# Kernel optimization log

Hardware: AMD Instinct MI355X
Metric: run time of the kernel (lower is better)

## Reference

```python
import jax, jax.numpy as jnp
import numpy as np
from jax import lax

B, T, I, H, G = 128, 1024, 256, 512, 4 * 512


def _lstm_layer(x, W_ih, W_hh, b_ih, b_hh):
    """x: [B, T, in]. Returns (outputs [B, T, H], final_h [B, H]).
    PyTorch gate order: i, f, g, o."""
    Bsz = x.shape[0]
    Hh = W_hh.shape[1]
    # Precompute input contribution to gates for all timesteps: [T, B, 4H]
    xg = jnp.einsum('bti,gi->tbg', x, W_ih) + b_ih + b_hh

    def step(carry, xg_t):
        h, c = carry
        g = xg_t + h @ W_hh.T  # [B, 4H]
        i, f, gg, o = jnp.split(g, 4, axis=-1)
        c = jax.nn.sigmoid(f) * c + jax.nn.sigmoid(i) * jnp.tanh(gg)
        h = jax.nn.sigmoid(o) * jnp.tanh(c)
        return (h, c), h

    zeros = jnp.zeros((Bsz, Hh), dtype=x.dtype)
    (h_T, _), hs = lax.scan(step, (zeros, zeros), xg)
    return jnp.transpose(hs, (1, 0, 2)), h_T


def setup_inputs() -> dict:
    key = jax.random.key(0)
    ks = jax.random.split(key, 11)
    s_in = 1.0 / np.sqrt(H)  # torch LSTM init scale ~ U(-1/sqrt(H), 1/sqrt(H))
    return {
        'x': jax.random.normal(ks[0], (B, T, I), jnp.float32),
        'W_ih0': jax.random.normal(ks[1], (G, I), jnp.float32) * s_in,
        'W_hh0': jax.random.normal(ks[2], (G, H), jnp.float32) * s_in,
        'b_ih0': jax.random.normal(ks[3], (G,), jnp.float32) * s_in,
        'b_hh0': jax.random.normal(ks[4], (G,), jnp.float32) * s_in,
        'W_ih1': jax.random.normal(ks[5], (G, H), jnp.float32) * s_in,
        'W_hh1': jax.random.normal(ks[6], (G, H), jnp.float32) * s_in,
        'b_ih1': jax.random.normal(ks[7], (G,), jnp.float32) * s_in,
        'b_hh1': jax.random.normal(ks[8], (G,), jnp.float32) * s_in,
        'fc_w': jax.random.normal(ks[9], (1, H), jnp.float32) * s_in,
        'fc_b': jax.random.normal(ks[10], (1,), jnp.float32) * s_in,
    }


def reference(x, W_ih0, W_hh0, b_ih0, b_hh0, W_ih1, W_hh1, b_ih1, b_hh1, fc_w, fc_b):
    out0, _ = _lstm_layer(x, W_ih0, W_hh0, b_ih0, b_hh0)
    _, h_last = _lstm_layer(out0, W_ih1, W_hh1, b_ih1, b_hh1)
    # dropout is identity in eval mode (and dropout=0.0)
    logits = h_last @ fc_w.T + fc_b  # [B, 1]
    return logits.squeeze(-1)  # [B]
```

## Files before the change

### kernel.cpp

```cpp
#include <hip/hip_runtime.h>
#include <stdint.h>


#define T_STEPS 1024
#define NBLK 512
#define NTHR 256

#define WS_WP0   0u
#define WS_WP1   3145728u
#define WS_BP0   7340032u
#define WS_BP1   7348224u
#define WS_H     7356416u
#define WS_CNT   8404992u
#define CNT_U32  512

typedef __bf16 bf16x8 __attribute__((ext_vector_type(8)));
typedef float  f32x4  __attribute__((ext_vector_type(4)));
typedef unsigned long long ull;
typedef ull u64x2 __attribute__((ext_vector_type(2)));

__device__ __forceinline__ unsigned short f2bf(float f) {
    union { float f; uint32_t u; } a; a.f = f;
    uint32_t r = a.u + 0x7fffu + ((a.u >> 16) & 1u);
    return (unsigned short)(r >> 16);
}
__device__ __forceinline__ float bf2f(unsigned short u) {
    union { uint32_t u; float f; } a; a.u = ((uint32_t)u) << 16; return a.f;
}
__device__ __forceinline__ float sigm(float x)  { return 1.f / (1.f + __expf(-x)); }
__device__ __forceinline__ float tanh_f(float x){ return 2.f / (1.f + __expf(-2.f * x)) - 1.f; }

__device__ __forceinline__ bf16x8 ld_h16(const unsigned short* p) {
    u64x2 t;
    t.x = __hip_atomic_load((const ull*)p,       __ATOMIC_RELAXED, __HIP_MEMORY_SCOPE_SYSTEM);
    t.y = __hip_atomic_load((const ull*)(p + 4), __ATOMIC_RELAXED, __HIP_MEMORY_SCOPE_SYSTEM);
    return __builtin_bit_cast(bf16x8, t);
}
__device__ __forceinline__ void st_sys_u32(unsigned* p, unsigned v) {
    __hip_atomic_store(p, v, __ATOMIC_RELAXED, __HIP_MEMORY_SCOPE_SYSTEM);
}
__device__ __forceinline__ unsigned ld_sys_u32(const unsigned* p) {
    return __hip_atomic_load(p, __ATOMIC_RELAXED, __HIP_MEMORY_SCOPE_SYSTEM);
}

__global__ void k_pack(const float* __restrict__ Wih0, const float* __restrict__ Whh0,
                       const float* __restrict__ Wih1, const float* __restrict__ Whh1,
                       unsigned short* __restrict__ Wp0, unsigned short* __restrict__ Wp1)
{
    int t = blockIdx.x * blockDim.x + threadIdx.x;
    const int N0 = 2048 * 768;
    const int N1 = 2048 * 1024;
    if (t < N0) {
        int r = t / 768, k = t - r * 768;
        int u = r >> 2, q = r & 3, row = q * 512 + u;
        float v = (k < 256) ? Wih0[row * 256 + k] : Whh0[row * 512 + (k - 256)];
        Wp0[t] = f2bf(v);
    } else if (t < N0 + N1) {
        int t2 = t - N0;
        int r = t2 >> 10, k = t2 & 1023;
        int u = r >> 2, q = r & 3, row = q * 512 + u;
        float v = (k < 512) ? Wih1[row * 512 + k] : Whh1[row * 512 + (k - 512)];
        Wp1[t2] = f2bf(v);
    }
}

__global__ void k_misc(const float* __restrict__ bih0, const float* __restrict__ bhh0,
                       const float* __restrict__ bih1, const float* __restrict__ bhh1,
                       float* __restrict__ bp0, float* __restrict__ bp1,
                       unsigned short* __restrict__ hbufs, unsigned* __restrict__ cnt)
{
    int t = blockIdx.x * blockDim.x + threadIdx.x;
    if (t < 2048) {
        int u = t >> 2, q = t & 3, row = q * 512 + u;
        bp0[t] = bih0[row] + bhh0[row];
    } else if (t < 4096) {
        int r = t - 2048; int u = r >> 2, q = r & 3, row = q * 512 + u;
        bp1[r] = bih1[row] + bhh1[row];
    } else if (t < 4096 + 524288) {
        hbufs[t - 4096] = 0;
    } else if (t < 4096 + 524288 + CNT_U32) {
        cnt[t - (4096 + 524288)] = 0;
    }
}

template<int NKW, int KTOT, int KS, bool L0>
__device__ __forceinline__ void run_layer(
    int b0, int ut0, int g0, int w, int col, int quad, int tid,
    const float* __restrict__ x,
    const unsigned short* __restrict__ Wp,
    const float* __restrict__ bp,
    unsigned short* __restrict__ hb,
    unsigned* slots, int myslot,
    float (*red)[16][68])
{
    const int bA   = b0 + col;
    const int lane = tid & 63;

    uint4 Bf[4][NKW];
    #pragma unroll
    for (int f = 0; f < 4; ++f) {
        const unsigned short* wrow = Wp + (g0 + f * 16 + col) * KTOT + w * (NKW * 32) + quad * 8;
        #pragma unroll
        for (int ks = 0; ks < NKW; ++ks)
            Bf[f][ks] = *(const uint4*)(wrow + ks * 32);
    }
    #pragma unroll
    for (int f = 0; f < 4; ++f) {
        #pragma unroll
        for (int ks = 0; ks < NKW; ++ks) {
            uint32_t c0 = Bf[f][ks].x, c1 = Bf[f][ks].y, c2 = Bf[f][ks].z, c3 = Bf[f][ks].w;
            asm volatile("" : "+v"(c0), "+v"(c1), "+v"(c2), "+v"(c3));
            Bf[f][ks].x = c0; Bf[f][ks].y = c1; Bf[f][ks].z = c2; Bf[f][ks].w = c3;
        }
    }

    const int bl = tid >> 4, ul = tid & 15;
    const f32x4 bias = *(const f32x4*)(bp + g0 + ul * 4);
    float c = 0.f;

    int  offA[NKW];
    bool s0[NKW];
    #pragma unroll
    for (int ks = 0; ks < NKW; ++ks) {
        int kg = w * (NKW * 32) + ks * 32 + quad * 8;
        if (kg < KS) { s0[ks] = true;  offA[ks] = L0 ? (bA * (T_STEPS * 256) + kg) : (bA * 512 + kg); }
        else         { s0[ks] = false; offA[ks] = bA * 512 + (kg - KS); }
    }

    const int SMAX = L0 ? (T_STEPS - 1) : T_STEPS;

    for (int s = 0; s <= SMAX; ++s) {
        const bool active = L0 || (s >= 1);
        bf16x8 Af[NKW];

        if (L0) {
            const float* xb = x + s * 256;
            #pragma unroll
            for (int ks = 0; ks < NKW; ++ks) {
                if (s0[ks]) {
                    const float* p = xb + offA[ks];
                    float4 lo = *(const float4*)p;
                    float4 hi = *(const float4*)(p + 4);
                    bf16x8 v;
                    v[0]=(__bf16)lo.x; v[1]=(__bf16)lo.y; v[2]=(__bf16)lo.z; v[3]=(__bf16)lo.w;
                    v[4]=(__bf16)hi.x; v[5]=(__bf16)hi.y; v[6]=(__bf16)hi.z; v[7]=(__bf16)hi.w;
                    Af[ks] = v;
                }
            }
        }

        if (s >= 1 && tid < 64) {
            int tgt = L0 ? (s - ((lane & 1) << 1)) : s;
            if (lane == myslot) tgt = (int)0x80000000;
            for (;;) {
                int v = (int)ld_sys_u32(slots + lane);
                if (__all(v >= tgt)) break;
                __builtin_amdgcn_s_sleep(1);
            }
        }
        __syncthreads();

        if (active) {
            if (L0) {
                const unsigned short* hr = hb + (((unsigned)(s + 3)) & 3u) * 65536;
                #pragma unroll
                for (int ks = 0; ks < NKW; ++ks)
                    if (!s0[ks]) Af[ks] = ld_h16(hr + offA[ks]);
            } else {
                const unsigned short* h0r = hb + (((unsigned)(s + 3)) & 3u) * 65536;
                const unsigned short* h1r = hb + 262144 + (((unsigned)(s + 2)) & 3u) * 65536;
                #pragma unroll
                for (int ks = 0; ks < NKW; ++ks)
                    Af[ks] = ld_h16((s0[ks] ? h0r : h1r) + offA[ks]);
            }

            f32x4 acc[4] = { f32x4{0,0,0,0}, f32x4{0,0,0,0}, f32x4{0,0,0,0}, f32x4{0,0,0,0} };
            #pragma unroll
            for (int ks = 0; ks < NKW; ++ks) {
                #pragma unroll
                for (int f = 0; f < 4; ++f)
                    acc[f] = __builtin_amdgcn_mfma_f32_16x16x32_bf16(
                        Af[ks], __builtin_bit_cast(bf16x8, Bf[f][ks]), acc[f], 0, 0, 0);
            }
            #pragma unroll
            for (int f = 0; f < 4; ++f) {
                #pragma unroll
                for (int r = 0; r < 4; ++r)
                    red[w][quad * 4 + r][f * 16 + col] = acc[f][r];
            }
        }
        __syncthreads();
        if (active) {
            f32x4 g = bias;
            #pragma unroll
            for (int ww = 0; ww < 4; ++ww)
                g += *(const f32x4*)&red[ww][bl][ul * 4];
            float ig = sigm(g[0]), fg = sigm(g[1]), gc = tanh_f(g[2]), og = sigm(g[3]);
            c = fg * c + ig * gc;
            float h = og * tanh_f(c);
            unsigned short hv = f2bf(h);
            unsigned short pv = (unsigned short)__shfl_xor((int)hv, 1);
            if (!(ul & 1)) {
                unsigned short* hw = L0
                    ? (hb + (((unsigned)s) & 3u) * 65536)
                    : (hb + 262144 + (((unsigned)(s + 3)) & 3u) * 65536);
                unsigned pk = (unsigned)hv | ((unsigned)pv << 16);
                st_sys_u32((unsigned*)(hw + (b0 + bl) * 512 + ut0 + ul), pk);
            }
        }
        asm volatile("s_waitcnt vmcnt(0)" ::: "memory");
        __syncthreads();
        if (tid == 0)
            st_sys_u32(slots + myslot, (unsigned)(s + 1));
    }
}

__global__ __launch_bounds__(NTHR, 2) void lstm_persistent(
    const float* __restrict__ x,
    const unsigned short* __restrict__ Wp0, const unsigned short* __restrict__ Wp1,
    const float* __restrict__ bp0, const float* __restrict__ bp1,
    unsigned short* __restrict__ hb, unsigned* __restrict__ cnt)
{
    __shared__ alignas(16) float red[4][16][68];
    const int bid   = blockIdx.x;
    const int g     = bid & 7;
    const int rest  = bid >> 3;
    const int layer = rest & 1;
    const int ut    = rest >> 1;
    const int b0    = g * 16;
    const int ut0   = ut * 16;
    const int g0    = ut * 64;
    const int tid   = threadIdx.x;
    const int w = tid >> 6, lane = tid & 63, col = lane & 15, quad = lane >> 4;

    unsigned* slots = cnt + g * 64;
    const int myslot = rest;

    if (layer == 0)
        run_layer<6, 768, 256, true >(b0, ut0, g0, w, col, quad, tid, x, Wp0, bp0, hb, slots, myslot, red);
    else
        run_layer<8, 1024, 512, false>(b0, ut0, g0, w, col, quad, tid, x, Wp1, bp1, hb, slots, myslot, red);
}

__global__ void k_fc(const unsigned short* __restrict__ h1, const float* __restrict__ fcw,
                     const float* __restrict__ fcb, float* __restrict__ out)
{
    int b = threadIdx.x;
    if (b < 128) {
        const unsigned short* hr = h1 + b * 512;
        float acc = 0.f;
        for (int u = 0; u < 512; ++u) acc += bf2f(hr[u]) * fcw[u];
        out[b] = acc + fcb[0];
    }
}

extern "C" void kernel_launch(void* const* d_in, const int* in_sizes, int n_in,
                              void* d_out, int out_size, void* d_ws, size_t ws_size,
                              hipStream_t stream)
{
    const float* x    = (const float*)d_in[0];
    const float* Wih0 = (const float*)d_in[1];
    const float* Whh0 = (const float*)d_in[2];
    const float* bih0 = (const float*)d_in[3];
    const float* bhh0 = (const float*)d_in[4];
    const float* Wih1 = (const float*)d_in[5];
    const float* Whh1 = (const float*)d_in[6];
    const float* bih1 = (const float*)d_in[7];
    const float* bhh1 = (const float*)d_in[8];
    const float* fcw  = (const float*)d_in[9];
    const float* fcb  = (const float*)d_in[10];

    char* ws = (char*)d_ws;
    unsigned short* Wp0 = (unsigned short*)(ws + WS_WP0);
    unsigned short* Wp1 = (unsigned short*)(ws + WS_WP1);
    float* bp0 = (float*)(ws + WS_BP0);
    float* bp1 = (float*)(ws + WS_BP1);
    unsigned short* hb = (unsigned short*)(ws + WS_H);
    unsigned* cnt = (unsigned*)(ws + WS_CNT);

    const int npack = 2048 * 768 + 2048 * 1024;
    k_pack<<<(npack + 255) / 256, 256, 0, stream>>>(Wih0, Whh0, Wih1, Whh1, Wp0, Wp1);
    const int nmisc = 4096 + 524288 + CNT_U32;
    k_misc<<<(nmisc + 255) / 256, 256, 0, stream>>>(bih0, bhh0, bih1, bhh1, bp0, bp1, hb, cnt);

    lstm_persistent<<<NBLK, NTHR, 0, stream>>>(x, Wp0, Wp1, bp0, bp1, hb, cnt);

    k_fc<<<1, 128, 0, stream>>>(hb + 262144 + 196608, fcw, fcb, (float*)d_out);
}
```

Baseline: 5.842 ms.

## Replace per-step block barriers with LDS token spin-waits and a dedicated gate wave

Drops two of the three __syncthreads per timestep and replaces them with volatile LDS tokens. Wave 0 polls the cross-block slots, and wave 1 alone computes the gate nonlinearities for all 16 batch rows, then publishes h and the slot counter. The reduction buffer is double-buffered by step parity so MFMA waves can start the next step while wave 1 is still finishing gates. The aim is to cut barrier latency on the serial recurrence. The cost is four times more serial element-wise work on one wave, plus busy-spinning on LDS.

Result: slower. 9.843 ms (+68.5%).

```diff
diff --git a/kernel.cpp b/kernel.cpp
--- a/kernel.cpp
+++ b/kernel.cpp
@@ -91,7 +91,7 @@
     const float* __restrict__ bp,
     unsigned short* __restrict__ hb,
     unsigned* slots, int myslot,
-    float (*red)[16][68])
+    float (*red)[4][16][68], volatile int* tok)
 {
     const int bA   = b0 + col;
     const int lane = tid & 63;
@@ -114,9 +114,9 @@
         }
     }
 
-    const int bl = tid >> 4, ul = tid & 15;
-    const f32x4 bias = *(const f32x4*)(bp + g0 + ul * 4);
-    float c = 0.f;
+    const int ul = lane & 15;
+    const f32x4 bias4 = *(const f32x4*)(bp + g0 + ul * 4);
+    float cst[4] = {0.f, 0.f, 0.f, 0.f};
 
     int  offA[NKW];
     bool s0[NKW];
@@ -149,16 +149,22 @@
             }
         }
 
-        if (s >= 1 && tid < 64) {
-            int tgt = L0 ? (s - ((lane & 1) << 1)) : s;
-            if (lane == myslot) tgt = (int)0x80000000;
-            for (;;) {
-                int v = (int)ld_sys_u32(slots + lane);
-                if (__all(v >= tgt)) break;
-                __builtin_amdgcn_s_sleep(1);
-            }
-        }
-        __syncthreads();
+        if (w == 0) {
+            if (s >= 1) {
+                int tgt = L0 ? (s - ((lane & 1) << 1)) : s;
+                if (lane == myslot) tgt = (int)0x80000000;
+                for (;;) {
+                    int v = (int)ld_sys_u32(slots + lane);
+                    if (__all(v >= tgt)) break;
+                    __builtin_amdgcn_s_sleep(1);
+                }
+            }
+            if (lane == 0) tok[0] = s;
+            while (tok[2] < s - 1) { }
+        } else {
+            while (tok[0] < s || tok[2] < s - 1) { }
+        }
+        asm volatile("" ::: "memory");
 
         if (active) {
             if (L0) {
@@ -182,36 +188,50 @@
                     acc[f] = __builtin_amdgcn_mfma_f32_16x16x32_bf16(
                         Af[ks], __builtin_bit_cast(bf16x8, Bf[f][ks]), acc[f], 0, 0, 0);
             }
+            while (tok[1] < s - 2) { }
+            asm volatile("" ::: "memory");
             #pragma unroll
             for (int f = 0; f < 4; ++f) {
                 #pragma unroll
                 for (int r = 0; r < 4; ++r)
-                    red[w][quad * 4 + r][f * 16 + col] = acc[f][r];
+                    red[s & 1][w][quad * 4 + r][f * 16 + col] = acc[f][r];
             }
         }
         __syncthreads();
-        if (active) {
-            f32x4 g = bias;
-            #pragma unroll
-            for (int ww = 0; ww < 4; ++ww)
-                g += *(const f32x4*)&red[ww][bl][ul * 4];
-            float ig = sigm(g[0]), fg = sigm(g[1]), gc = tanh_f(g[2]), og = sigm(g[3]);
-            c = fg * c + ig * gc;
-            float h = og * tanh_f(c);
-            unsigned short hv = f2bf(h);
-            unsigned short pv = (unsigned short)__shfl_xor((int)hv, 1);
-            if (!(ul & 1)) {
+
+        if (w == 1) {
+            if (active) {
+                unsigned pk[4];
+                #pragma unroll
+                for (int k = 0; k < 4; ++k) {
+                    const int bl = (lane >> 4) + 4 * k;
+                    f32x4 g = bias4;
+                    #pragma unroll
+                    for (int ww = 0; ww < 4; ++ww)
+                        g += *(const f32x4*)&red[s & 1][ww][bl][ul * 4];
+                    float ig = sigm(g[0]), fg = sigm(g[1]), gc = tanh_f(g[2]), og = sigm(g[3]);
+                    cst[k] = fg * cst[k] + ig * gc;
+                    float h = og * tanh_f(cst[k]);
+                    unsigned hv = (unsigned)f2bf(h);
+                    unsigned pv = (unsigned)__shfl_xor((int)hv, 1);
+                    pk[k] = hv | (pv << 16);
+                }
+                if (lane == 0) tok[1] = s;
                 unsigned short* hw = L0
                     ? (hb + (((unsigned)s) & 3u) * 65536)
                     : (hb + 262144 + (((unsigned)(s + 3)) & 3u) * 65536);
-                unsigned pk = (unsigned)hv | ((unsigned)pv << 16);
-                st_sys_u32((unsigned*)(hw + (b0 + bl) * 512 + ut0 + ul), pk);
-            }
-        }
-        asm volatile("s_waitcnt vmcnt(0)" ::: "memory");
-        __syncthreads();
-        if (tid == 0)
-            st_sys_u32(slots + myslot, (unsigned)(s + 1));
+                if (!(ul & 1)) {
+                    #pragma unroll
+                    for (int k = 0; k < 4; ++k) {
+                        const int bl = (lane >> 4) + 4 * k;
+                        st_sys_u32((unsigned*)(hw + (b0 + bl) * 512 + ut0 + ul), pk[k]);
+                    }
+                }
+                asm volatile("s_waitcnt vmcnt(0)" ::: "memory");
+            }
+            if (lane == 0) { tok[2] = s; }
+            if (lane == 0) st_sys_u32(slots + myslot, (unsigned)(s + 1));
+        }
     }
 }
 
@@ -221,7 +241,8 @@
     const float* __restrict__ bp0, const float* __restrict__ bp1,
     unsigned short* __restrict__ hb, unsigned* __restrict__ cnt)
 {
-    __shared__ alignas(16) float red[4][16][68];
+    __shared__ alignas(16) float red[2][4][16][68];
+    __shared__ int tokbuf[4];
     const int bid   = blockIdx.x;
     const int g     = bid & 7;
     const int rest  = bid >> 3;
@@ -233,13 +254,17 @@
     const int tid   = threadIdx.x;
     const int w = tid >> 6, lane = tid & 63, col = lane & 15, quad = lane >> 4;
 
+    if (tid == 0) { tokbuf[0] = -1; tokbuf[1] = -1; tokbuf[2] = -1; tokbuf[3] = 0; }
+    __syncthreads();
+    volatile int* tok = tokbuf;
+
     unsigned* slots = cnt + g * 64;
     const int myslot = rest;
 
     if (layer == 0)
-        run_layer<6, 768, 256, true >(b0, ut0, g0, w, col, quad, tid, x, Wp0, bp0, hb, slots, myslot, red);
+        run_layer<6, 768, 256, true >(b0, ut0, g0, w, col, quad, tid, x, Wp0, bp0, hb, slots, myslot, red, tok);
     else
-        run_layer<8, 1024, 512, false>(b0, ut0, g0, w, col, quad, tid, x, Wp1, bp1, hb, slots, myslot, red);
+        run_layer<8, 1024, 512, false>(b0, ut0, g0, w, col, quad, tid, x, Wp1, bp1, hb, slots, myslot, red, tok);
 }
 
 __global__ void k_fc(const unsigned short* __restrict__ h1, const float* __restrict__ fcw,
```
